# Kernel optimization log

Measured on AMD Instinct MI355X. Metric: run time of the kernel, lower is better.

Reference implementation:

```python
import jax, jax.numpy as jnp
import numpy as np

B, T, F, H, L = 128, 256, 128, 768, 2


def lstm_cell(x, h, c, Wih, Whh, b):
    # torch gate order: i, f, g, o
    gates = x @ Wih.T + h @ Whh.T + b
    i, f, g, o = jnp.split(gates, 4, axis=-1)
    i = jax.nn.sigmoid(i)
    f = jax.nn.sigmoid(f)
    g = jnp.tanh(g)
    o = jax.nn.sigmoid(o)
    c2 = f * c + i * g
    h2 = o * jnp.tanh(c2)
    return h2, c2


def setup_inputs() -> dict:
    key = jax.random.key(0)
    ks = jax.random.split(key, 20)
    k_scale = 1.0 / np.sqrt(H)

    def U(k, shape):
        return jax.random.uniform(k, shape, jnp.float32, -k_scale, k_scale)

    inp = {
        "x": jax.random.normal(ks[0], (B, T, F), jnp.float32),
        "h0": jax.random.normal(ks[1], (L, B, H), jnp.float32),
        "c0": jax.random.normal(ks[2], (L, B, H), jnp.float32),
        # encoder LSTM (layer 0 input dim F, layer 1 input dim H); b = b_ih + b_hh fused
        "enc_Wih0": U(ks[3], (4 * H, F)),
        "enc_Whh0": U(ks[4], (4 * H, H)),
        "enc_b0": U(ks[5], (4 * H,)),
        "enc_Wih1": U(ks[6], (4 * H, H)),
        "enc_Whh1": U(ks[7], (4 * H, H)),
        "enc_b1": U(ks[8], (4 * H,)),
        # decoder LSTM
        "dec_Wih0": U(ks[9], (4 * H, F)),
        "dec_Whh0": U(ks[10], (4 * H, H)),
        "dec_b0": U(ks[11], (4 * H,)),
        "dec_Wih1": U(ks[12], (4 * H, H)),
        "dec_Whh1": U(ks[13], (4 * H, H)),
        "dec_b1": U(ks[14], (4 * H,)),
        # output projection hidden -> feature
        "lin_W": U(ks[15], (F, H)),
        "lin_b": U(ks[16], (F,)),
    }
    return inp


def reference(x, h0, c0,
              enc_Wih0, enc_Whh0, enc_b0, enc_Wih1, enc_Whh1, enc_b1,
              dec_Wih0, dec_Whh0, dec_b0, dec_Wih1, dec_Whh1, dec_b1,
              lin_W, lin_b):
    # ---- Encoder: 2-layer LSTM over full sequence, keep final (h, c) ----
    xs = jnp.transpose(x, (1, 0, 2))  # [T, B, F]

    def enc_step(carry, xt):
        (h_l0, h_l1), (c_l0, c_l1) = carry
        h0n, c0n = lstm_cell(xt, h_l0, c_l0, enc_Wih0, enc_Whh0, enc_b0)
        h1n, c1n = lstm_cell(h0n, h_l1, c_l1, enc_Wih1, enc_Whh1, enc_b1)
        return ((h0n, h1n), (c0n, c1n)), None

    enc_init = ((h0[0], h0[1]), (c0[0], c0[1]))
    (h_fin, c_fin), _ = jax.lax.scan(enc_step, enc_init, xs)

    x_dec0 = x[:, -1, :]  # [B, F]

    def dec_step(carry, _):
        (h_l0, h_l1), (c_l0, c_l1), xd = carry
        h0n, c0n = lstm_cell(xd, h_l0, c_l0, dec_Wih0, dec_Whh0, dec_b0)
        h1n, c1n = lstm_cell(h0n, h_l1, c_l1, dec_Wih1, dec_Whh1, dec_b1)
        y = h1n @ lin_W.T + lin_b  # [B, F]
        return (((h0n, h1n), (c0n, c1n), y)), y

    dec_init = (h_fin, c_fin, x_dec0)
    _, ys = jax.lax.scan(dec_step, dec_init, None, length=T)  # [T, B, F]

    # decoder step t writes output index T-1-t -> reversed time order
    out = jnp.transpose(jnp.flip(ys, axis=0), (1, 0, 2))  # [B, T, F]
    return out
```

## Files before the change

kernel.cpp:

```cpp
#include <hip/hip_runtime.h>

#define B_ 128
#define T_ 256
#define F_ 128
#define H_ 768
#define NG 3072
#define BM 32
#define BN 64
#define BK 128
#define UPT 16

typedef short s16x8 __attribute__((ext_vector_type(8)));
typedef float f32x4 __attribute__((ext_vector_type(4)));

__device__ __forceinline__ unsigned short f2bf(float x) {
  unsigned u = __float_as_uint(x);
  u += 0x7fffu + ((u >> 16) & 1u);
  return (unsigned short)(u >> 16);
}

__device__ __forceinline__ void async16(const void* g, void* l) {
  __builtin_amdgcn_global_load_lds(
      (const __attribute__((address_space(1))) void*)g,
      (__attribute__((address_space(3))) void*)l, 16, 0, 0);
}

struct Cell {
  const unsigned short* A1; int lda1; int K1;
  const unsigned short* A2; int lda2; int K2;
  const unsigned short* W;  int ldw;
  const float* bias;
  float* c;
  unsigned short* h;
  float* yout; int yt;
  int N; int ngates;
};

__device__ __forceinline__ void compute_frag(const char* At, const char* Bt,
                                             f32x4 acc[2], int wm, int wn, int lane) {
#pragma unroll
  for (int ks = 0; ks < 4; ++ks) {
    int ar = wm*16 + (lane & 15);
    int as = (ks*4 + (lane >> 4)) ^ (ar & 7);
    s16x8 a = *(const s16x8*)(At + ar*256 + as*16);
#pragma unroll
    for (int nf = 0; nf < 2; ++nf) {
      int br = wn*32 + nf*16 + (lane & 15);
      int bsl = (ks*4 + (lane >> 4)) ^ (br & 7);
      s16x8 b = *(const s16x8*)(Bt + br*256 + bsl*16);
      acc[nf] = __builtin_amdgcn_mfma_f32_16x16x32_bf16(a, b, acc[nf], 0, 0, 0);
    }
  }
}

__global__ __launch_bounds__(256, 2) void enc_kernel(Cell ca, Cell cb, int mode)
{
  __shared__ union SM {
    struct { unsigned short A[3][BM*BK]; unsigned short Bm[3][BN*BK]; } stg;
    float gates[BM][BN+4];
  } sm;

  const int bid = (int)blockIdx.x;
  int tm, tn; bool isB = false;
  if (mode == 0) {
    int xcd = bid & 7, j = bid >> 3;
    isB = j >= 24; int jj = isB ? j - 24 : j;
    tn = xcd * 6 + (jj >> 2); tm = jj & 3;
  } else if (mode == 2) {
    int xcd = bid & 7, j = bid >> 3;
    tn = xcd * 6 + (j >> 2); tm = j & 3;
  } else {
    tm = bid & 3; tn = bid >> 2;
  }
  const Cell C = isB ? cb : ca;
  const int b0 = tm * BM;

  const int tid  = (int)threadIdx.x;
  const int wave = tid >> 6;
  const int lane = tid & 63;
  const int wm = wave >> 1, wn = wave & 1;

  const int nit = (C.K1 + C.K2) / BK;

  f32x4 acc[2] = {{0.f,0.f,0.f,0.f},{0.f,0.f,0.f,0.f}};

  auto stage = [&](int buf, int ck) {
    int kk = ck * BK;
#pragma unroll
    for (int q = 0; q < 2; ++q) {
      int cch = wave*2 + q;
      int P = cch*1024 + lane*16;
      int r = P >> 8;
      int sl = ((P >> 4) & 15) ^ (r & 7);
      int ke = kk + sl*8;
      const unsigned short* gp = (ke < C.K1)
        ? (C.A1 + (long)(b0 + r) * C.lda1 + ke)
        : (C.A2 + (long)(b0 + r) * C.lda2 + (ke - C.K1));
      async16(gp, (char*)(sm.stg.A[buf]) + cch*1024);
    }
#pragma unroll
    for (int q = 0; q < 4; ++q) {
      int cch = wave*4 + q;
      int P = cch*1024 + lane*16;
      int r = P >> 8;
      int sl = ((P >> 4) & 15) ^ (r & 7);
      int ke = kk + sl*8;
      const unsigned short* gp = C.W + (long)(tn*BN + r) * C.ldw + ke;
      async16(gp, (char*)(sm.stg.Bm[buf]) + cch*1024);
    }
  };

  stage(0, 0);
  stage(1, 1);
  for (int it = 0; it < nit; ++it) {
    if (it + 1 < nit) asm volatile("s_waitcnt vmcnt(6)" ::: "memory");
    else              asm volatile("s_waitcnt vmcnt(0)" ::: "memory");
    __builtin_amdgcn_s_barrier();
    __builtin_amdgcn_sched_barrier(0);
    if (it + 2 < nit) stage((it + 2) % 3, it + 2);
    compute_frag((const char*)sm.stg.A[it % 3], (const char*)sm.stg.Bm[it % 3],
                 acc, wm, wn, lane);
  }

  const int gcol0 = tn * BN;
  if (gcol0 >= C.ngates) {
#pragma unroll
    for (int nf = 0; nf < 2; ++nf) {
      int col = wn*32 + nf*16 + (lane & 15);
      float bia = C.bias[gcol0 + col];
      int fo = gcol0 + col - C.ngates;
#pragma unroll
      for (int rg = 0; rg < 4; ++rg) {
        int brow = wm*16 + (lane >> 4)*4 + rg;
        C.yout[(long)(b0 + brow)*(T_*F_) + (long)C.yt*F_ + fo] = acc[nf][rg] + bia;
      }
    }
    return;
  }

  __syncthreads();
#pragma unroll
  for (int nf = 0; nf < 2; ++nf) {
    int col = wn*32 + nf*16 + (lane & 15);
#pragma unroll
    for (int rg = 0; rg < 4; ++rg) {
      int brow = wm*16 + (lane >> 4)*4 + rg;
      sm.gates[brow][col] = acc[nf][rg];
    }
  }
  __syncthreads();

  const float* bs0 = C.bias + (long)tn*BN;
  for (int e = tid; e < BM*UPT; e += 256) {
    int bl = e >> 4, ul = e & 15;
    float gi = sm.gates[bl][ 0 + ul] + bs0[ 0 + ul];
    float gf = sm.gates[bl][16 + ul] + bs0[16 + ul];
    float gg = sm.gates[bl][32 + ul] + bs0[32 + ul];
    float go = sm.gates[bl][48 + ul] + bs0[48 + ul];
    float iv = 1.f / (1.f + __expf(-gi));
    float fv = 1.f / (1.f + __expf(-gf));
    float gc = fminf(fmaxf(gg, -15.f), 15.f);
    float eg = __expf(2.f * gc);
    float gv = (eg - 1.f) / (eg + 1.f);
    float ov = 1.f / (1.f + __expf(-go));
    long ci = (long)(b0 + bl)*H_ + (long)tn*UPT + ul;
    float c2 = fv * C.c[ci] + iv * gv;
    C.c[ci] = c2;
    float cc = fminf(fmaxf(c2, -15.f), 15.f);
    float ec = __expf(2.f * cc);
    float th = (ec - 1.f) / (ec + 1.f);
    C.h[ci] = f2bf(ov * th);
  }
}

__global__ __launch_bounds__(256, 1) void dec_kernel(Cell C, int mode)
{
  __shared__ struct SMD {
    char A[12][8192];
    char Bm[3][16384];
    float ctile[BM][UPT];
    float gates[BM][BN+4];
  } sm;

  const int bid = (int)blockIdx.x;
  const int tid = (int)threadIdx.x;
  const int wave = tid >> 6, lane = tid & 63;
  const int wm = wave >> 1, wn = wave & 1;

  int tm, tn;
  if (mode == 1) {
    int xcd = bid & 7, j = bid >> 3;
    if (j < 24) { tn = xcd*6 + (j >> 2); tm = j & 3; }
    else        { tn = 48 + (xcd >> 2); tm = xcd & 3; }
  } else {
    int xcd = bid & 7, j = bid >> 3;
    tn = xcd*6 + (j >> 2); tm = j & 3;
  }
  const int b0 = tm * BM;
  const int nit = (C.K1 + C.K2) / BK;
  const int gcol0 = tn * BN;
  const bool hasC = (C.c != nullptr) && (gcol0 < C.ngates);

  if (hasC) {
    int off = (wave & 1) * 1024 + lane * 16;
    int r = off >> 6, cc = (off & 63) >> 2;
    async16(C.c + (long)(b0 + r) * H_ + (long)tn * UPT + cc,
            &sm.ctile[r][cc]);
  }

  for (int ck = 0; ck < nit; ++ck) {
    int kk = ck * BK;
#pragma unroll
    for (int q = 0; q < 2; ++q) {
      int cch = wave*2 + q;
      int P = cch*1024 + lane*16;
      int r = P >> 8;
      int sl = ((P >> 4) & 15) ^ (r & 7);
      int ke = kk + sl*8;
      const unsigned short* gp = (ke < C.K1)
        ? (C.A1 + (long)(b0 + r) * C.lda1 + ke)
        : (C.A2 + (long)(b0 + r) * C.lda2 + (ke - C.K1));
      async16(gp, sm.A[ck] + cch*1024);
    }
  }

  auto stageB = [&](int buf, int ck) {
    int kk = ck * BK;
#pragma unroll
    for (int q = 0; q < 4; ++q) {
      int cch = wave*4 + q;
      int P = cch*1024 + lane*16;
      int r = P >> 8;
      int sl = ((P >> 4) & 15) ^ (r & 7);
      int ke = kk + sl*8;
      async16(C.W + (long)(tn*BN + r) * C.ldw + ke, sm.Bm[buf] + cch*1024);
    }
  };
  stageB(0, 0);
  if (nit > 1) stageB(1, 1);

  f32x4 acc[2] = {{0.f,0.f,0.f,0.f},{0.f,0.f,0.f,0.f}};
  for (int it = 0; it < nit; ++it) {
    if (it + 1 < nit) asm volatile("s_waitcnt vmcnt(4)" ::: "memory");
    else              asm volatile("s_waitcnt vmcnt(0)" ::: "memory");
    __builtin_amdgcn_s_barrier();
    __builtin_amdgcn_sched_barrier(0);
    if (it + 2 < nit) stageB((it + 2) % 3, it + 2);
    compute_frag(sm.A[it], sm.Bm[it % 3], acc, wm, wn, lane);
  }

  if (gcol0 >= C.ngates) {
#pragma unroll
    for (int nf = 0; nf < 2; ++nf) {
      int col = wn*32 + nf*16 + (lane & 15);
      float bia = C.bias[gcol0 + col];
      int fo = gcol0 + col - C.ngates;
#pragma unroll
      for (int rg = 0; rg < 4; ++rg) {
        int brow = wm*16 + (lane >> 4)*4 + rg;
        C.yout[(long)(b0 + brow)*(T_*F_) + (long)C.yt*F_ + fo] = acc[nf][rg] + bia;
      }
    }
    return;
  }

  __syncthreads();
#pragma unroll
  for (int nf = 0; nf < 2; ++nf) {
    int col = wn*32 + nf*16 + (lane & 15);
#pragma unroll
    for (int rg = 0; rg < 4; ++rg) {
      int brow = wm*16 + (lane >> 4)*4 + rg;
      sm.gates[brow][col] = acc[nf][rg];
    }
  }
  __syncthreads();

  const float* bs0 = C.bias + (long)tn*BN;
  for (int e = tid; e < BM*UPT; e += 256) {
    int bl = e >> 4, ul = e & 15;
    float gi = sm.gates[bl][ 0 + ul] + bs0[ 0 + ul];
    float gf = sm.gates[bl][16 + ul] + bs0[16 + ul];
    float gg = sm.gates[bl][32 + ul] + bs0[32 + ul];
    float go = sm.gates[bl][48 + ul] + bs0[48 + ul];
    float iv = 1.f / (1.f + __expf(-gi));
    float fv = 1.f / (1.f + __expf(-gf));
    float gc = fminf(fmaxf(gg, -15.f), 15.f);
    float eg = __expf(2.f * gc);
    float gv = (eg - 1.f) / (eg + 1.f);
    float ov = 1.f / (1.f + __expf(-go));
    long ci = (long)(b0 + bl)*H_ + (long)tn*UPT + ul;
    float c2 = fv * sm.ctile[bl][ul] + iv * gv;
    C.c[ci] = c2;
    float cc = fminf(fmaxf(c2, -15.f), 15.f);
    float ec = __expf(2.f * cc);
    float th = (ec - 1.f) / (ec + 1.f);
    C.h[ci] = f2bf(ov * th);
  }
}

__global__ void k_convx(const float* x, unsigned short* xbf, long n) {
  long st = (long)gridDim.x * 256;
  for (long i = (long)blockIdx.x*256 + threadIdx.x; i < n; i += st) xbf[i] = f2bf(x[i]);
}

__global__ void k_init(const float* h0in, const float* c0in,
                       unsigned short* h0e0, unsigned short* h1e1,
                       float* c0buf, float* c1buf) {
  int i = blockIdx.x*256 + threadIdx.x;
  if (i < B_*H_) {
    h0e0[i] = f2bf(h0in[i]);
    h1e1[i] = f2bf(h0in[B_*H_ + i]);
    c0buf[i] = c0in[i];
    c1buf[i] = c0in[B_*H_ + i];
  }
}

__global__ __launch_bounds__(256) void k_wcomb(const float* A, const float* Bm, float* Cm) {
  __shared__ float sA[16*128];
  int tid = threadIdx.x;
  int r0 = blockIdx.x * 16;
  int c0 = blockIdx.y * 128;
  for (int e = tid; e < 16*128; e += 256)
    sA[e] = A[(long)(r0 + (e >> 7))*128 + (e & 127)];
  __syncthreads();
  int col = c0 + (tid & 127);
  int rg = (tid >> 7) * 8;
  float acc[8] = {0,0,0,0,0,0,0,0};
  for (int k = 0; k < 128; ++k) {
    float b = Bm[(long)k*768 + col];
#pragma unroll
    for (int r = 0; r < 8; ++r) acc[r] += sA[(rg + r)*128 + k] * b;
  }
  for (int r = 0; r < 8; ++r) Cm[(long)(r0 + rg + r)*768 + col] = acc[r];
}

__global__ void k_bcomb(const float* dWih0, const float* linb, const float* db0, float* bc) {
  int j = blockIdx.x*256 + threadIdx.x;
  if (j < NG) {
    float s = db0[j];
    for (int f = 0; f < 128; ++f) s += dWih0[(long)j*128 + f] * linb[f];
    bc[j] = s;
  }
}

__global__ void k_pack(unsigned short* dst, float* bdst, const float* s1, int K1,
                       const float* s2, int K2, const float* bs) {
  long Kt = K1 + K2, total = (long)NG * Kt;
  long st = (long)gridDim.x * 256;
  for (long i = (long)blockIdx.x*256 + threadIdx.x; i < total; i += st) {
    int n = (int)(i / Kt), k = (int)(i % Kt);
    int tn = n >> 6, r = n & 63;
    int j = (r >> 4)*H_ + tn*UPT + (r & 15);
    float v = (k < K1) ? s1[(long)j*K1 + k] : s2[(long)j*K2 + (k - K1)];
    dst[i] = f2bf(v);
    if (k == 0) bdst[n] = bs[j];
  }
}

__global__ void k_packext(unsigned short* dst, float* bdst, const float* wcomb,
                          const float* whh0, const float* bcomb,
                          const float* linW, const float* linb) {
  long total = (long)(NG + F_) * (2*H_);
  long st = (long)gridDim.x * 256;
  for (long i = (long)blockIdx.x*256 + threadIdx.x; i < total; i += st) {
    int n = (int)(i / (2*H_)), k = (int)(i % (2*H_));
    float v;
    if (n < NG) {
      int tn = n >> 6, r = n & 63;
      int j = (r >> 4)*H_ + tn*UPT + (r & 15);
      v = (k < H_) ? wcomb[(long)j*H_ + k] : whh0[(long)j*H_ + (k - H_)];
      if (k == 0) bdst[n] = bcomb[j];
    } else {
      int f = n - NG;
      v = (k < H_) ? linW[(long)f*H_ + k] : 0.f;
      if (k == 0) bdst[n] = linb[f];
    }
    dst[i] = f2bf(v);
  }
}

__global__ void k_packlin(unsigned short* dst, const float* linW) {
  int i = blockIdx.x*256 + threadIdx.x;
  if (i < F_*H_) dst[i] = f2bf(linW[i]);
}

extern "C" void kernel_launch(void* const* d_in, const int* in_sizes, int n_in,
                              void* d_out, int out_size, void* d_ws, size_t ws_size,
                              hipStream_t stream)
{
  (void)in_sizes; (void)n_in; (void)out_size; (void)ws_size;
  const float* x     = (const float*)d_in[0];
  const float* h0in  = (const float*)d_in[1];
  const float* c0in  = (const float*)d_in[2];
  const float* eWih0 = (const float*)d_in[3];
  const float* eWhh0 = (const float*)d_in[4];
  const float* eb0   = (const float*)d_in[5];
  const float* eWih1 = (const float*)d_in[6];
  const float* eWhh1 = (const float*)d_in[7];
  const float* eb1   = (const float*)d_in[8];
  const float* dWih0 = (const float*)d_in[9];
  const float* dWhh0 = (const float*)d_in[10];
  const float* db0   = (const float*)d_in[11];
  const float* dWih1 = (const float*)d_in[12];
  const float* dWhh1 = (const float*)d_in[13];
  const float* db1   = (const float*)d_in[14];
  const float* linW  = (const float*)d_in[15];
  const float* linb  = (const float*)d_in[16];
  float* out = (float*)d_out;

  char* wp = (char*)d_ws;
  auto alloc = [&](size_t bytes) -> void* {
    void* p = (void*)wp;
    wp += (bytes + 255) & ~(size_t)255;
    return p;
  };
  unsigned short* xbf    = (unsigned short*)alloc((size_t)B_*T_*F_*2);
  unsigned short* Wenc0  = (unsigned short*)alloc((size_t)NG*(F_+H_)*2);
  unsigned short* Wenc1  = (unsigned short*)alloc((size_t)NG*(2*H_)*2);
  unsigned short* Wdec0f = (unsigned short*)alloc((size_t)NG*(F_+H_)*2);
  unsigned short* Wext   = (unsigned short*)alloc((size_t)(NG+F_)*(2*H_)*2);
  unsigned short* Wdec1  = (unsigned short*)alloc((size_t)NG*(2*H_)*2);
  unsigned short* linWbf = (unsigned short*)alloc((size_t)F_*H_*2);
  float* Wcomb = (float*)alloc((size_t)NG*H_*4);
  float* benc0 = (float*)alloc((size_t)NG*4);
  float* benc1 = (float*)alloc((size_t)NG*4);
  float* bdec0f= (float*)alloc((size_t)NG*4);
  float* bext  = (float*)alloc((size_t)(NG+F_)*4);
  float* bdec1 = (float*)alloc((size_t)NG*4);
  float* bcomb = (float*)alloc((size_t)NG*4);
  unsigned short* h0e[2];
  h0e[0] = (unsigned short*)alloc((size_t)B_*H_*2);
  h0e[1] = (unsigned short*)alloc((size_t)B_*H_*2);
  unsigned short* h1e[2];
  h1e[0] = (unsigned short*)alloc((size_t)B_*H_*2);
  h1e[1] = (unsigned short*)alloc((size_t)B_*H_*2);
  float* c0buf = (float*)alloc((size_t)B_*H_*4);
  float* c1buf = (float*)alloc((size_t)B_*H_*4);

  k_convx<<<2048, 256, 0, stream>>>(x, xbf, (long)B_*T_*F_);
  k_init<<<(B_*H_+255)/256, 256, 0, stream>>>(h0in, c0in, h0e[0], h1e[1], c0buf, c1buf);
  k_wcomb<<<dim3(192,6), 256, 0, stream>>>(dWih0, linW, Wcomb);
  k_bcomb<<<(NG+255)/256, 256, 0, stream>>>(dWih0, linb, db0, bcomb);
  k_pack<<<2048, 256, 0, stream>>>(Wenc0, benc0, eWih0, F_, eWhh0, H_, eb0);
  k_pack<<<2048, 256, 0, stream>>>(Wenc1, benc1, eWih1, H_, eWhh1, H_, eb1);
  k_pack<<<2048, 256, 0, stream>>>(Wdec0f, bdec0f, dWih0, F_, dWhh0, H_, db0);
  k_pack<<<2048, 256, 0, stream>>>(Wdec1, bdec1, dWih1, H_, dWhh1, H_, db1);
  k_packext<<<2048, 256, 0, stream>>>(Wext, bext, Wcomb, dWhh0, bcomb, linW, linb);
  k_packlin<<<(F_*H_+255)/256, 256, 0, stream>>>(linWbf, linW);

  auto mk = [&](const unsigned short* A1, int lda1, int K1,
                const unsigned short* A2, int lda2, int K2,
                const unsigned short* W, const float* bias,
                float* c, unsigned short* h, float* yo, int yt,
                int N, int ngates) {
    Cell cc; cc.A1=A1; cc.lda1=lda1; cc.K1=K1; cc.A2=A2; cc.lda2=lda2; cc.K2=K2;
    cc.W=W; cc.ldw=K1+K2; cc.bias=bias; cc.c=c; cc.h=h; cc.yout=yo; cc.yt=yt;
    cc.N=N; cc.ngates=ngates;
    return cc;
  };

  for (int s = 0; s <= T_; ++s) {
    Cell cA = {}, cB = {};
    bool hasA = (s < T_), hasB = (s >= 1);
    if (hasA)
      cA = mk(xbf + (long)s*F_, T_*F_, F_, h0e[s&1], H_, H_,
              Wenc0, benc0, c0buf, h0e[(s+1)&1], nullptr, 0, NG, NG);
    if (hasB)
      cB = mk(h0e[s&1], H_, H_, h1e[s&1], H_, H_,
              Wenc1, benc1, c1buf, h1e[(s+1)&1], nullptr, 0, NG, NG);
    if (hasA && hasB) enc_kernel<<<384, 256, 0, stream>>>(cA, cB, 0);
    else if (hasA)    enc_kernel<<<192, 256, 0, stream>>>(cA, cA, 2);
    else              enc_kernel<<<192, 256, 0, stream>>>(cB, cB, 2);
  }

  {
    Cell c0f = mk(xbf + (long)(T_-1)*F_, T_*F_, F_, h0e[0], H_, H_,
                  Wdec0f, bdec0f, c0buf, h0e[1], nullptr, 0, NG, NG);
    dec_kernel<<<192, 256, 0, stream>>>(c0f, 2);
    Cell c10 = mk(h0e[1], H_, H_, h1e[1], H_, H_,
                  Wdec1, bdec1, c1buf, h1e[0], nullptr, 0, NG, NG);
    dec_kernel<<<192, 256, 0, stream>>>(c10, 2);
  }
  for (int t = 1; t < T_; ++t) {
    Cell cd0 = mk(h1e[(t+1)&1], H_, H_, h0e[t&1], H_, H_,
                  Wext, bext, c0buf, h0e[(t+1)&1], out, T_-t, NG+F_, NG);
    dec_kernel<<<200, 256, 0, stream>>>(cd0, 1);
    Cell cd1 = mk(h0e[(t+1)&1], H_, H_, h1e[(t+1)&1], H_, H_,
                  Wdec1, bdec1, c1buf, h1e[t&1], nullptr, 0, NG, NG);
    dec_kernel<<<192, 256, 0, stream>>>(cd1, 2);
  }
  {
    Cell cy = mk(h1e[1], H_, H_, h1e[1], H_, 0,
                 linWbf, linb, nullptr, nullptr, out, 0, F_, 0);
    enc_kernel<<<8, 256, 0, stream>>>(cy, cy, 3);
  }
}
```

Measured before the change: 7.051 ms.

## Fuse decoder time loop into one persistent kernel with grid barriers

Replaces the 512-odd per-step decoder kernel launches with a single persistent kernel of 200 blocks that loops over all decoder phases. Blocks synchronize between phases through a software grid barrier: each block sets an arrival flag, and block 0 collects them and publishes a release flag. This removes per-launch overhead and the implicit launch gaps. It adds spin-wait latency on a centralized barrier and depends on all 200 blocks being co-resident, with a timeout abort as a safety net.

Measured after the change: 10.92 ms. 1.55x slower.

```diff
diff --git a/kernel.cpp b/kernel.cpp
--- a/kernel.cpp
+++ b/kernel.cpp
@@ -9,6 +9,7 @@
 #define BN 64
 #define BK 128
 #define UPT 16
+#define NB 200
 
 typedef short s16x8 __attribute__((ext_vector_type(8)));
 typedef float f32x4 __attribute__((ext_vector_type(4)));
@@ -173,129 +174,230 @@
   }
 }
 
-__global__ __launch_bounds__(256, 1) void dec_kernel(Cell C, int mode)
+struct DecP {
+  const unsigned short *xbf, *Wdec0f, *Wext, *Wdec1, *linWbf;
+  const float *bdec0f, *bext, *bdec1, *linb;
+  unsigned short *h00, *h01, *h10, *h11;
+  float *c0, *c1;
+  float* out;
+  int* arr;
+  int* rel;
+  int* abortf;
+};
+
+__global__ __launch_bounds__(256, 1) void dec_persist(DecP P)
 {
-  __shared__ struct SMD {
+  __shared__ struct {
     char A[12][8192];
-    char Bm[3][16384];
-    float ctile[BM][UPT];
-    float gates[BM][BN+4];
+    union { char Bm[3][16384]; float gates[BM][BN+4]; } u;
   } sm;
+  __shared__ int sres;
 
   const int bid = (int)blockIdx.x;
   const int tid = (int)threadIdx.x;
   const int wave = tid >> 6, lane = tid & 63;
   const int wm = wave >> 1, wn = wave & 1;
 
-  int tm, tn;
-  if (mode == 1) {
-    int xcd = bid & 7, j = bid >> 3;
-    if (j < 24) { tn = xcd*6 + (j >> 2); tm = j & 3; }
-    else        { tn = 48 + (xcd >> 2); tm = xcd & 3; }
-  } else {
-    int xcd = bid & 7, j = bid >> 3;
-    tn = xcd*6 + (j >> 2); tm = j & 3;
-  }
-  const int b0 = tm * BM;
-  const int nit = (C.K1 + C.K2) / BK;
-  const int gcol0 = tn * BN;
-  const bool hasC = (C.c != nullptr) && (gcol0 < C.ngates);
-
-  if (hasC) {
-    int off = (wave & 1) * 1024 + lane * 16;
-    int r = off >> 6, cc = (off & 63) >> 2;
-    async16(C.c + (long)(b0 + r) * H_ + (long)tn * UPT + cc,
-            &sm.ctile[r][cc]);
-  }
-
-  for (int ck = 0; ck < nit; ++ck) {
-    int kk = ck * BK;
-#pragma unroll
-    for (int q = 0; q < 2; ++q) {
-      int cch = wave*2 + q;
-      int P = cch*1024 + lane*16;
-      int r = P >> 8;
-      int sl = ((P >> 4) & 15) ^ (r & 7);
-      int ke = kk + sl*8;
-      const unsigned short* gp = (ke < C.K1)
-        ? (C.A1 + (long)(b0 + r) * C.lda1 + ke)
-        : (C.A2 + (long)(b0 + r) * C.lda2 + (ke - C.K1));
-      async16(gp, sm.A[ck] + cch*1024);
-    }
-  }
-
-  auto stageB = [&](int buf, int ck) {
-    int kk = ck * BK;
-#pragma unroll
-    for (int q = 0; q < 4; ++q) {
-      int cch = wave*4 + q;
-      int P = cch*1024 + lane*16;
-      int r = P >> 8;
-      int sl = ((P >> 4) & 15) ^ (r & 7);
-      int ke = kk + sl*8;
-      async16(C.W + (long)(tn*BN + r) * C.ldw + ke, sm.Bm[buf] + cch*1024);
-    }
-  };
-  stageB(0, 0);
-  if (nit > 1) stageB(1, 1);
-
-  f32x4 acc[2] = {{0.f,0.f,0.f,0.f},{0.f,0.f,0.f,0.f}};
-  for (int it = 0; it < nit; ++it) {
-    if (it + 1 < nit) asm volatile("s_waitcnt vmcnt(4)" ::: "memory");
-    else              asm volatile("s_waitcnt vmcnt(0)" ::: "memory");
-    __builtin_amdgcn_s_barrier();
-    __builtin_amdgcn_sched_barrier(0);
-    if (it + 2 < nit) stageB((it + 2) % 3, it + 2);
-    compute_frag(sm.A[it], sm.Bm[it % 3], acc, wm, wn, lane);
-  }
-
-  if (gcol0 >= C.ngates) {
-#pragma unroll
-    for (int nf = 0; nf < 2; ++nf) {
-      int col = wn*32 + nf*16 + (lane & 15);
-      float bia = C.bias[gcol0 + col];
-      int fo = gcol0 + col - C.ngates;
-#pragma unroll
-      for (int rg = 0; rg < 4; ++rg) {
-        int brow = wm*16 + (lane >> 4)*4 + rg;
-        C.yout[(long)(b0 + brow)*(T_*F_) + (long)C.yt*F_ + fo] = acc[nf][rg] + bia;
-      }
-    }
-    return;
-  }
-
-  __syncthreads();
-#pragma unroll
-  for (int nf = 0; nf < 2; ++nf) {
-    int col = wn*32 + nf*16 + (lane & 15);
-#pragma unroll
-    for (int rg = 0; rg < 4; ++rg) {
-      int brow = wm*16 + (lane >> 4)*4 + rg;
-      sm.gates[brow][col] = acc[nf][rg];
-    }
-  }
-  __syncthreads();
-
-  const float* bs0 = C.bias + (long)tn*BN;
-  for (int e = tid; e < BM*UPT; e += 256) {
-    int bl = e >> 4, ul = e & 15;
-    float gi = sm.gates[bl][ 0 + ul] + bs0[ 0 + ul];
-    float gf = sm.gates[bl][16 + ul] + bs0[16 + ul];
-    float gg = sm.gates[bl][32 + ul] + bs0[32 + ul];
-    float go = sm.gates[bl][48 + ul] + bs0[48 + ul];
-    float iv = 1.f / (1.f + __expf(-gi));
-    float fv = 1.f / (1.f + __expf(-gf));
-    float gc = fminf(fmaxf(gg, -15.f), 15.f);
-    float eg = __expf(2.f * gc);
-    float gv = (eg - 1.f) / (eg + 1.f);
-    float ov = 1.f / (1.f + __expf(-go));
-    long ci = (long)(b0 + bl)*H_ + (long)tn*UPT + ul;
-    float c2 = fv * sm.ctile[bl][ul] + iv * gv;
-    C.c[ci] = c2;
-    float cc = fminf(fmaxf(c2, -15.f), 15.f);
-    float ec = __expf(2.f * cc);
-    float th = (ec - 1.f) / (ec + 1.f);
-    C.h[ci] = f2bf(ov * th);
+  const int xcd = bid & 7, j = bid >> 3;
+  const bool isGate = (j < 24);
+  const int tmg = isGate ? (j & 3) : 0;
+  const int tng = isGate ? (xcd * 6 + (j >> 2)) : 0;
+  const int tmy = xcd & 3, tny = 48 + (xcd >> 2);
+
+  unsigned short* h0e[2] = { P.h00, P.h01 };
+  unsigned short* h1e[2] = { P.h10, P.h11 };
+
+  for (int p = 0; p <= 512; ++p) {
+    const unsigned short *A1 = nullptr, *A2 = nullptr, *W = nullptr;
+    const float* bias = nullptr;
+    float* cst = nullptr; unsigned short* hdst = nullptr;
+    float* yout = nullptr; int yt = 0;
+    long lda1 = 0, lda2 = 0; int K1 = 0, K2 = 0, ldw = 0, ngates = 0;
+    int tm = tmg, tn = tng;
+    bool active = false;
+
+    if (p == 512) {
+      if (bid < 8) {
+        active = true; tm = bid & 3; tn = bid >> 2;
+        A1 = h1e[1]; lda1 = H_; K1 = H_; K2 = 0;
+        W = P.linWbf; ldw = H_;
+        bias = P.linb; ngates = 0;
+        yout = P.out; yt = 0;
+      }
+    } else if ((p & 1) == 0) {
+      int t = p >> 1;
+      if (t == 0) {
+        if (isGate) {
+          active = true;
+          A1 = P.xbf + (long)(T_-1)*F_; lda1 = (long)T_*F_; K1 = F_;
+          A2 = h0e[0]; lda2 = H_; K2 = H_;
+          W = P.Wdec0f; ldw = F_+H_;
+          bias = P.bdec0f; ngates = NG;
+          cst = P.c0; hdst = h0e[1];
+        }
+      } else {
+        active = true;
+        if (!isGate) { tm = tmy; tn = tny; }
+        A1 = h1e[(t+1)&1]; lda1 = H_; K1 = H_;
+        A2 = h0e[t&1];     lda2 = H_; K2 = H_;
+        W = P.Wext; ldw = 2*H_;
+        bias = P.bext; ngates = NG;
+        cst = P.c0; hdst = h0e[(t+1)&1];
+        yout = P.out; yt = T_ - t;
+      }
+    } else {
+      int t = (p - 1) >> 1;
+      if (isGate) {
+        active = true;
+        if (t == 0) { A1 = h0e[1]; A2 = h1e[1]; hdst = h1e[0]; }
+        else        { A1 = h0e[(t+1)&1]; A2 = h1e[(t+1)&1]; hdst = h1e[t&1]; }
+        lda1 = H_; K1 = H_; lda2 = H_; K2 = H_;
+        W = P.Wdec1; ldw = 2*H_;
+        bias = P.bdec1; ngates = NG;
+        cst = P.c1;
+      }
+    }
+
+    if (active) {
+      const int b0 = tm * BM;
+      const int nit = (K1 + K2) / BK;
+      const int gcol0 = tn * BN;
+
+      for (int ck = 0; ck < nit; ++ck) {
+        int kk = ck * BK;
+#pragma unroll
+        for (int q = 0; q < 2; ++q) {
+          int cch = wave*2 + q;
+          int Pb = cch*1024 + lane*16;
+          int r = Pb >> 8;
+          int sl = ((Pb >> 4) & 15) ^ (r & 7);
+          int ke = kk + sl*8;
+          const unsigned short* gp = (ke < K1)
+            ? (A1 + (long)(b0 + r) * lda1 + ke)
+            : (A2 + (long)(b0 + r) * lda2 + (ke - K1));
+          async16(gp, sm.A[ck] + cch*1024);
+        }
+      }
+      auto stageB = [&](int buf, int ck) {
+        int kk = ck * BK;
+#pragma unroll
+        for (int q = 0; q < 4; ++q) {
+          int cch = wave*4 + q;
+          int Pb = cch*1024 + lane*16;
+          int r = Pb >> 8;
+          int sl = ((Pb >> 4) & 15) ^ (r & 7);
+          int ke = kk + sl*8;
+          async16(W + (long)(tn*BN + r) * ldw + ke, sm.u.Bm[buf] + cch*1024);
+        }
+      };
+      stageB(0, 0);
+      if (nit > 1) stageB(1, 1);
+
+      f32x4 acc[2] = {{0.f,0.f,0.f,0.f},{0.f,0.f,0.f,0.f}};
+      for (int it = 0; it < nit; ++it) {
+        if (it + 1 < nit) asm volatile("s_waitcnt vmcnt(4)" ::: "memory");
+        else              asm volatile("s_waitcnt vmcnt(0)" ::: "memory");
+        __builtin_amdgcn_s_barrier();
+        __builtin_amdgcn_sched_barrier(0);
+        if (it + 2 < nit) stageB((it + 2) % 3, it + 2);
+        compute_frag(sm.A[it], sm.u.Bm[it % 3], acc, wm, wn, lane);
+      }
+
+      if (gcol0 >= ngates) {
+#pragma unroll
+        for (int nf = 0; nf < 2; ++nf) {
+          int col = wn*32 + nf*16 + (lane & 15);
+          float bia = bias[gcol0 + col];
+          int fo = gcol0 + col - ngates;
+#pragma unroll
+          for (int rg = 0; rg < 4; ++rg) {
+            int brow = wm*16 + (lane >> 4)*4 + rg;
+            yout[(long)(b0 + brow)*(T_*F_) + (long)yt*F_ + fo] = acc[nf][rg] + bia;
+          }
+        }
+      } else {
+        __syncthreads();
+#pragma unroll
+        for (int nf = 0; nf < 2; ++nf) {
+          int col = wn*32 + nf*16 + (lane & 15);
+#pragma unroll
+          for (int rg = 0; rg < 4; ++rg) {
+            int brow = wm*16 + (lane >> 4)*4 + rg;
+            sm.u.gates[brow][col] = acc[nf][rg];
+          }
+        }
+        __syncthreads();
+        const float* bs0 = bias + (long)tn*BN;
+        for (int e = tid; e < BM*UPT; e += 256) {
+          int bl = e >> 4, ul = e & 15;
+          float gi = sm.u.gates[bl][ 0 + ul] + bs0[ 0 + ul];
+          float gf = sm.u.gates[bl][16 + ul] + bs0[16 + ul];
+          float gg = sm.u.gates[bl][32 + ul] + bs0[32 + ul];
+          float go = sm.u.gates[bl][48 + ul] + bs0[48 + ul];
+          float iv = 1.f / (1.f + __expf(-gi));
+          float fv = 1.f / (1.f + __expf(-gf));
+          float gc = fminf(fmaxf(gg, -15.f), 15.f);
+          float eg = __expf(2.f * gc);
+          float gv = (eg - 1.f) / (eg + 1.f);
+          float ov = 1.f / (1.f + __expf(-go));
+          long ci = (long)(b0 + bl)*H_ + (long)tn*UPT + ul;
+          float c2 = fv * cst[ci] + iv * gv;
+          cst[ci] = c2;
+          float cc2 = fminf(fmaxf(c2, -15.f), 15.f);
+          float ec = __expf(2.f * cc2);
+          float th = (ec - 1.f) / (ec + 1.f);
+          hdst[ci] = f2bf(ov * th);
+        }
+      }
+    }
+
+    if (p < 512) {
+      __syncthreads();
+      if (tid == 0) {
+        __hip_atomic_store(P.arr + p*256 + bid, 1, __ATOMIC_RELEASE, __HIP_MEMORY_SCOPE_AGENT);
+        sres = 1;
+      }
+      __syncthreads();
+      if (bid == 0) {
+        if (tid < NB) {
+          bool ok = true; int n = 0;
+          while (__hip_atomic_load(P.arr + p*256 + tid, __ATOMIC_RELAXED, __HIP_MEMORY_SCOPE_AGENT) == 0) {
+            __builtin_amdgcn_s_sleep(2);
+            if ((++n & 127) == 0) {
+              if (__hip_atomic_load(P.abortf, __ATOMIC_RELAXED, __HIP_MEMORY_SCOPE_AGENT)) { ok = false; break; }
+              if (n > 400000) {
+                __hip_atomic_store(P.abortf, 1, __ATOMIC_RELAXED, __HIP_MEMORY_SCOPE_AGENT);
+                ok = false; break;
+              }
+            }
+          }
+          if (ok) (void)__hip_atomic_load(P.arr + p*256 + tid, __ATOMIC_ACQUIRE, __HIP_MEMORY_SCOPE_AGENT);
+          else sres = 0;
+        }
+        __syncthreads();
+        if (tid == 0 && sres)
+          __hip_atomic_store(P.rel + p, 1, __ATOMIC_RELEASE, __HIP_MEMORY_SCOPE_AGENT);
+        if (!sres) return;
+      } else {
+        if (tid == 0) {
+          int ok = 1, n = 0;
+          while (__hip_atomic_load(P.rel + p, __ATOMIC_RELAXED, __HIP_MEMORY_SCOPE_AGENT) == 0) {
+            __builtin_amdgcn_s_sleep(4);
+            if ((++n & 127) == 0) {
+              if (__hip_atomic_load(P.abortf, __ATOMIC_RELAXED, __HIP_MEMORY_SCOPE_AGENT)) { ok = 0; break; }
+              if (n > 400000) {
+                __hip_atomic_store(P.abortf, 1, __ATOMIC_RELAXED, __HIP_MEMORY_SCOPE_AGENT);
+                ok = 0; break;
+              }
+            }
+          }
+          if (ok) (void)__hip_atomic_load(P.rel + p, __ATOMIC_ACQUIRE, __HIP_MEMORY_SCOPE_AGENT);
+          sres = ok;
+        }
+        __syncthreads();
+        if (!sres) return;
+      }
+    }
   }
 }
 
@@ -415,6 +517,11 @@
     wp += (bytes + 255) & ~(size_t)255;
     return p;
   };
+  const size_t nsync = (size_t)513*256 + 513 + 16;
+  int* syncmem = (int*)alloc(nsync * 4);
+  int* arr = syncmem;
+  int* rel = syncmem + 513*256;
+  int* abortf = rel + 513;
   unsigned short* xbf    = (unsigned short*)alloc((size_t)B_*T_*F_*2);
   unsigned short* Wenc0  = (unsigned short*)alloc((size_t)NG*(F_+H_)*2);
   unsigned short* Wenc1  = (unsigned short*)alloc((size_t)NG*(2*H_)*2);
@@ -438,6 +545,8 @@
   float* c0buf = (float*)alloc((size_t)B_*H_*4);
   float* c1buf = (float*)alloc((size_t)B_*H_*4);
 
+  hipMemsetAsync(syncmem, 0, nsync * 4, stream);
+
   k_convx<<<2048, 256, 0, stream>>>(x, xbf, (long)B_*T_*F_);
   k_init<<<(B_*H_+255)/256, 256, 0, stream>>>(h0in, c0in, h0e[0], h1e[1], c0buf, c1buf);
   k_wcomb<<<dim3(192,6), 256, 0, stream>>>(dWih0, linW, Wcomb);
@@ -474,25 +583,12 @@
     else              enc_kernel<<<192, 256, 0, stream>>>(cB, cB, 2);
   }
 
-  {
-    Cell c0f = mk(xbf + (long)(T_-1)*F_, T_*F_, F_, h0e[0], H_, H_,
-                  Wdec0f, bdec0f, c0buf, h0e[1], nullptr, 0, NG, NG);
-    dec_kernel<<<192, 256, 0, stream>>>(c0f, 2);
-    Cell c10 = mk(h0e[1], H_, H_, h1e[1], H_, H_,
-                  Wdec1, bdec1, c1buf, h1e[0], nullptr, 0, NG, NG);
-    dec_kernel<<<192, 256, 0, stream>>>(c10, 2);
-  }
-  for (int t = 1; t < T_; ++t) {
-    Cell cd0 = mk(h1e[(t+1)&1], H_, H_, h0e[t&1], H_, H_,
-                  Wext, bext, c0buf, h0e[(t+1)&1], out, T_-t, NG+F_, NG);
-    dec_kernel<<<200, 256, 0, stream>>>(cd0, 1);
-    Cell cd1 = mk(h0e[(t+1)&1], H_, H_, h1e[(t+1)&1], H_, H_,
-                  Wdec1, bdec1, c1buf, h1e[t&1], nullptr, 0, NG, NG);
-    dec_kernel<<<192, 256, 0, stream>>>(cd1, 2);
-  }
-  {
-    Cell cy = mk(h1e[1], H_, H_, h1e[1], H_, 0,
-                 linWbf, linb, nullptr, nullptr, out, 0, F_, 0);
-    enc_kernel<<<8, 256, 0, stream>>>(cy, cy, 3);
-  }
-}
+  DecP P;
+  P.xbf = xbf; P.Wdec0f = Wdec0f; P.Wext = Wext; P.Wdec1 = Wdec1; P.linWbf = linWbf;
+  P.bdec0f = bdec0f; P.bext = bext; P.bdec1 = bdec1; P.linb = linb;
+  P.h00 = h0e[0]; P.h01 = h0e[1]; P.h10 = h1e[0]; P.h11 = h1e[1];
+  P.c0 = c0buf; P.c1 = c1buf;
+  P.out = out;
+  P.arr = arr; P.rel = rel; P.abortf = abortf;
+  dec_persist<<<NB, 256, 0, stream>>>(P);
+}
```
